# Optimization experiments

Measured on AMD Instinct MI355X. Metric: run time of the kernel, lower is better.

Reference implementation:

```python
import jax, jax.numpy as jnp
import numpy as np

NUM_EMBEDDINGS = 1024
EMBEDDING_DIM = 256
COMMITMENT_COST = 0.25


def setup_inputs() -> dict:
    key = jax.random.key(0)
    kx, ke = jax.random.split(key)
    x = jax.random.normal(kx, (8, EMBEDDING_DIM, 16, 32, 32), dtype=jnp.float32)
    emb = jax.random.uniform(ke, (NUM_EMBEDDINGS, EMBEDDING_DIM), dtype=jnp.float32,
                             minval=-1.0 / NUM_EMBEDDINGS, maxval=1.0 / NUM_EMBEDDINGS)
    return {"x": x, "emb": emb}


def reference(x, emb):
    sg = jax.lax.stop_gradient
    # x: [B, C, T, H, W] -> channels-last [B, T, H, W, C]
    x_flat = jnp.transpose(x, (0, 2, 3, 4, 1))
    flat = x_flat.reshape(-1, EMBEDDING_DIM)  # [N, D]
    # squared L2 distances to each codeword: [N, K]
    distances = (jnp.sum(flat ** 2, axis=1, keepdims=True)
                 + jnp.sum(emb ** 2, axis=1)
                 - 2.0 * flat @ emb.T)
    encoding_indices = jnp.argmin(distances, axis=1)  # [N]
    # one-hot @ codebook == direct gather
    quantized = emb[encoding_indices].reshape(x_flat.shape)
    loss = (jnp.mean((sg(quantized) - x_flat) ** 2)
            + COMMITMENT_COST * jnp.mean((quantized - sg(x_flat)) ** 2))
    # straight-through estimator
    quantized_st = x_flat + sg(quantized - x_flat)
    return jnp.transpose(quantized_st, (0, 4, 1, 2, 3)), loss
```

## Files before the change

kernel.cpp:

```cpp
#include <hip/hip_runtime.h>
#include <hip/hip_bf16.h>
#include <stdint.h>

#define N_TOT    131072
#define DIM      256
#define KCODES   1024
#define THW      16384
#define OUT_ELEMS 33554432ULL

typedef short short8 __attribute__((ext_vector_type(8)));
typedef float f32x4  __attribute__((ext_vector_type(4)));

__device__ __forceinline__ unsigned short f2bf_rne(float f) {
  union { float f; unsigned int u; } c; c.f = f;
  unsigned int u = c.u;
  unsigned int r = u + 0x7FFFu + ((u >> 16) & 1u);
  return (unsigned short)(r >> 16);
}

__device__ __forceinline__ void async_cp16(void* lds, const void* gsrc) {
  __builtin_amdgcn_global_load_lds(
      (const __attribute__((address_space(1))) void*)gsrc,
      (__attribute__((address_space(3))) void*)lds, 16, 0, 0);
}

__global__ __launch_bounds__(64) void k_prep(const float* __restrict__ emb,
                                             unsigned short* __restrict__ embB,
                                             float* __restrict__ e2) {
  const int k = blockIdx.x;
  const int t = threadIdx.x;
  const float4 v = ((const float4*)(emb + (size_t)k * DIM))[t];
  float s = v.x * v.x + v.y * v.y + v.z * v.z + v.w * v.w;
  ushort4 bv;
  bv.x = f2bf_rne(v.x); bv.y = f2bf_rne(v.y);
  bv.z = f2bf_rne(v.z); bv.w = f2bf_rne(v.w);
  const int c0 = 4 * t;
  const int ks = c0 >> 5, q = (c0 >> 3) & 3, j0 = c0 & 7;
  const int lane = q * 16 + (k & 15);
  unsigned short* dst = embB + (size_t)((((k >> 4) * 8 + ks) * 64 + lane) * 8 + j0);
  *(ushort4*)dst = bv;
  #pragma unroll
  for (int m = 32; m; m >>= 1) s += __shfl_xor(s, m, 64);
  if (t == 0) e2[k] = s;
}

__global__ __launch_bounds__(256) void k_gemm_argmin(
    const float* __restrict__ x, const unsigned short* __restrict__ embB,
    const float* __restrict__ e2, int* __restrict__ idxOut,
    float* __restrict__ lossPart) {
  __shared__ __align__(16) unsigned short eT[2][8192];
  __shared__ __align__(16) float e2l[KCODES];
  __shared__ float red[4];

  const int tid  = threadIdx.x;
  const int wave = tid >> 6;
  const int lane = tid & 63;
  const int q    = lane >> 4;
  const int l15  = lane & 15;
  const int nw0  = blockIdx.x * 128 + wave * 32;
  const int b    = nw0 >> 14;

  async_cp16((char*)e2l + tid * 16, (const char*)e2 + tid * 16);
  {
    const char* gsrc = (const char*)embB;
    char* ldst = (char*)&eT[0][0];
    #pragma unroll
    for (int kk = 0; kk < 4; ++kk)
      async_cp16(ldst + (tid + kk * 256) * 16, gsrc + (size_t)(tid + kk * 256) * 16);
  }

  short8 A[2][8];
  float x2sum = 0.0f;
  #pragma unroll
  for (int mf = 0; mf < 2; ++mf) {
    const int n   = nw0 + mf * 16 + l15;
    const int thw = n & (THW - 1);
    const float* __restrict__ xr = x + (size_t)b * DIM * THW + thw;
    #pragma unroll
    for (int ks = 0; ks < 8; ++ks) {
      const int c0 = ks * 32 + q * 8;
      short8 a;
      #pragma unroll
      for (int j = 0; j < 8; ++j) {
        float v = xr[(size_t)(c0 + j) * THW];
        x2sum += v * v;
        a[j] = (short)f2bf_rne(-2.0f * v);
      }
      A[mf][ks] = a;
    }
  }

  float pmin[2][4];
  #pragma unroll
  for (int mf = 0; mf < 2; ++mf)
    #pragma unroll
    for (int r = 0; r < 4; ++r) pmin[mf][r] = 3.4e38f;

  __syncthreads();

  for (int ch = 0; ch < 32; ++ch) {
    if (ch + 1 < 32) {
      const char* gsrc = (const char*)embB + (size_t)(ch + 1) * 16384;
      char* ldst = (char*)&eT[(ch + 1) & 1][0];
      #pragma unroll
      for (int kk = 0; kk < 4; ++kk)
        async_cp16(ldst + (tid + kk * 256) * 16, gsrc + (size_t)(tid + kk * 256) * 16);
    }
    const unsigned short* __restrict__ buf = &eT[ch & 1][0];
    const int cb = ch * 32;

    #pragma unroll
    for (int cgl = 0; cgl < 2; ++cgl) {
      short8 B[8];
      #pragma unroll
      for (int ks = 0; ks < 8; ++ks)
        B[ks] = *(const short8*)(buf + (size_t)(((cgl * 8 + ks) * 64 + lane) * 8));
      const int   cod = cb + cgl * 16 + l15;
      const float e2v = e2l[cod];

      f32x4 acc0 = {0.f, 0.f, 0.f, 0.f};
      f32x4 acc1 = {0.f, 0.f, 0.f, 0.f};
      #pragma unroll
      for (int ks = 0; ks < 8; ++ks) {
        acc0 = __builtin_amdgcn_mfma_f32_16x16x32_bf16(A[0][ks], B[ks], acc0, 0, 0, 0);
        acc1 = __builtin_amdgcn_mfma_f32_16x16x32_bf16(A[1][ks], B[ks], acc1, 0, 0, 0);
      }
      const unsigned int codu = (unsigned int)cod;
      #pragma unroll
      for (int r = 0; r < 4; ++r) {
        float d0 = acc0[r] + e2v;
        unsigned int u0 = (__float_as_uint(d0) & 0xFFFFFC00u) | codu;
        pmin[0][r] = fminf(pmin[0][r], __uint_as_float(u0));
        float d1 = acc1[r] + e2v;
        unsigned int u1 = (__float_as_uint(d1) & 0xFFFFFC00u) | codu;
        pmin[1][r] = fminf(pmin[1][r], __uint_as_float(u1));
      }
    }
    __syncthreads();
  }

  #pragma unroll
  for (int m = 1; m <= 8; m <<= 1)
    #pragma unroll
    for (int mf = 0; mf < 2; ++mf)
      #pragma unroll
      for (int r = 0; r < 4; ++r)
        pmin[mf][r] = fminf(pmin[mf][r], __shfl_xor(pmin[mf][r], m, 64));

  float sstar = 0.0f;
  if (l15 == 0) {
    #pragma unroll
    for (int mf = 0; mf < 2; ++mf)
      #pragma unroll
      for (int r = 0; r < 4; ++r) {
        const unsigned int u = __float_as_uint(pmin[mf][r]);
        idxOut[nw0 + mf * 16 + q * 4 + r] = (int)(u & 1023u);
        sstar += __uint_as_float(u & 0xFFFFFC00u);
      }
  }
  float tot = x2sum + sstar;
  #pragma unroll
  for (int m = 32; m; m >>= 1) tot += __shfl_xor(tot, m, 64);
  if (lane == 0) red[wave] = tot;
  __syncthreads();
  if (tid == 0) lossPart[blockIdx.x] = red[0] + red[1] + red[2] + red[3];
}

#define TSTR 33
__global__ __launch_bounds__(256) void k_out(
    const float* __restrict__ emb, const int* __restrict__ idx,
    float* __restrict__ out, const float* __restrict__ lossPart) {
  __shared__ __align__(16) float tile[256 * TSTR];
  const int tid  = threadIdx.x;
  const int wave = tid >> 6;
  const int lane = tid & 63;
  const int l15  = lane & 15;
  const int n0   = blockIdx.x * 256;

  if (blockIdx.x == 0 && tid < 64) {
    float s = 0.0f;
    #pragma unroll
    for (int i = 0; i < 16; ++i) s += lossPart[tid + i * 64];
    #pragma unroll
    for (int m = 32; m; m >>= 1) s += __shfl_xor(s, m, 64);
    if (tid == 0) out[OUT_ELEMS] = 1.25f * s * (1.0f / (float)OUT_ELEMS);
  }

  const int myid = idx[n0 + tid];
  const int b    = n0 >> 14;
  const int thw0 = n0 & (THW - 1);
  float* __restrict__ ob = out + (size_t)b * DIM * THW + thw0;
  const float* __restrict__ er = emb + (size_t)myid * DIM;

  for (int cc = 0; cc < 8; ++cc) {
    const int c0 = cc * 32;
    #pragma unroll
    for (int j = 0; j < 8; ++j) {
      const float4 v = *(const float4*)(er + c0 + 4 * j);
      *(float4*)&tile[tid * TSTR + 4 * j] = v;
    }
    __syncthreads();
    #pragma unroll
    for (int ci = 0; ci < 8; ++ci) {
      const int dc = (lane >> 4) + 4 * ci;
      const int nl = wave * 64 + 4 * l15;
      float4 v;
      v.x = tile[(nl + 0) * TSTR + dc];
      v.y = tile[(nl + 1) * TSTR + dc];
      v.z = tile[(nl + 2) * TSTR + dc];
      v.w = tile[(nl + 3) * TSTR + dc];
      *(float4*)(ob + (size_t)(c0 + dc) * THW + nl) = v;
    }
    __syncthreads();
  }
}

extern "C" void kernel_launch(void* const* d_in, const int* in_sizes, int n_in,
                              void* d_out, int out_size, void* d_ws, size_t ws_size,
                              hipStream_t stream) {
  const float* x   = (const float*)d_in[0];
  const float* emb = (const float*)d_in[1];
  float* out = (float*)d_out;
  char* ws = (char*)d_ws;

  unsigned short* embB = (unsigned short*)(ws);
  float* e2      = (float*)(ws + 524288);
  int*   idx     = (int*)(ws + 528384);
  float* lossPart = (float*)(ws + 1052672);

  k_prep<<<KCODES, 64, 0, stream>>>(emb, embB, e2);
  k_gemm_argmin<<<N_TOT / 128, 256, 0, stream>>>(x, embB, e2, idx, lossPart);
  k_out<<<N_TOT / 256, 256, 0, stream>>>(emb, idx, out, lossPart);
}
```

Baseline: 370.7 us.

## Pre-convert x to bf16 MFMA fragment layout in separate kernel, use output as scratch

Adds a k_xprep kernel that reads x with coalesced float4 loads, converts it to bf16 (scaled by -2), transposes it through LDS into the MFMA A-fragment layout, and stores it into the output buffer as scratch. It also computes the x^2 partial sums. The GEMM kernel then loads its A fragments with 16-byte vector reads instead of strided scalar float loads. B fragments are now loaded inside the ks loop to lower register pressure, and k_out stages 64 channels per LDS tile instead of 32. The cost is an extra kernel launch plus a round trip of bf16 x through global memory, and k_out uses more shared memory per block.

```diff
diff --git a/kernel.cpp b/kernel.cpp
--- a/kernel.cpp
+++ b/kernel.cpp
@@ -44,8 +44,66 @@
   if (t == 0) e2[k] = s;
 }
 
+__global__ __launch_bounds__(1024) void k_xprep(const float* __restrict__ x,
+                                                unsigned short* __restrict__ xf,
+                                                float* __restrict__ lossPartX) {
+  __shared__ __align__(16) unsigned short sm[64 * 264];
+  __shared__ float xred[16];
+  const int tid  = threadIdx.x;
+  const int w    = tid >> 6;
+  const int l    = tid & 63;
+  const int n0   = blockIdx.x << 8;
+  const int b    = n0 >> 14;
+  const int thw0 = n0 & (THW - 1);
+  const float* __restrict__ xb = x + (size_t)b * DIM * THW;
+  float x2 = 0.0f;
+
+  for (int q4 = 0; q4 < 4; ++q4) {
+    ushort4 bv[4];
+    #pragma unroll
+    for (int i = 0; i < 4; ++i) {
+      const int c = q4 * 64 + w * 4 + i;
+      const float4 v = *(const float4*)(xb + (size_t)c * THW + thw0 + 4 * l);
+      x2 += v.x * v.x + v.y * v.y + v.z * v.z + v.w * v.w;
+      bv[i].x = f2bf_rne(-2.0f * v.x); bv[i].y = f2bf_rne(-2.0f * v.y);
+      bv[i].z = f2bf_rne(-2.0f * v.z); bv[i].w = f2bf_rne(-2.0f * v.w);
+    }
+    if (q4) __syncthreads();
+    #pragma unroll
+    for (int i = 0; i < 4; ++i) {
+      const int cc = w * 4 + i;
+      *(ushort4*)&sm[cc * 264 + 4 * l] = bv[i];
+    }
+    __syncthreads();
+    const int oo = tid >> 7;
+    const int t2 = tid & 127;
+    unsigned int r[8];
+    #pragma unroll
+    for (int j = 0; j < 8; ++j)
+      r[j] = *(const unsigned int*)&sm[(oo * 8 + j) * 264 + 2 * t2];
+    uint4 u0, u1;
+    u0.x = (r[0] & 0xFFFFu) | (r[1] << 16);  u1.x = (r[0] >> 16) | (r[1] & 0xFFFF0000u);
+    u0.y = (r[2] & 0xFFFFu) | (r[3] << 16);  u1.y = (r[2] >> 16) | (r[3] & 0xFFFF0000u);
+    u0.z = (r[4] & 0xFFFFu) | (r[5] << 16);  u1.z = (r[4] >> 16) | (r[5] & 0xFFFF0000u);
+    u0.w = (r[6] & 0xFFFFu) | (r[7] << 16);  u1.w = (r[6] >> 16) | (r[7] & 0xFFFF0000u);
+    const size_t ui = ((size_t)blockIdx.x * 32 + (size_t)(q4 * 8 + oo)) * 256 + 2 * t2;
+    ((uint4*)xf)[ui]     = u0;
+    ((uint4*)xf)[ui + 1] = u1;
+  }
+  #pragma unroll
+  for (int m = 32; m; m >>= 1) x2 += __shfl_xor(x2, m, 64);
+  if (l == 0) xred[w] = x2;
+  __syncthreads();
+  if (tid == 0) {
+    float s = 0.0f;
+    #pragma unroll
+    for (int i = 0; i < 16; ++i) s += xred[i];
+    lossPartX[blockIdx.x] = s;
+  }
+}
+
 __global__ __launch_bounds__(256) void k_gemm_argmin(
-    const float* __restrict__ x, const unsigned short* __restrict__ embB,
+    const unsigned short* __restrict__ xf, const unsigned short* __restrict__ embB,
     const float* __restrict__ e2, int* __restrict__ idxOut,
     float* __restrict__ lossPart) {
   __shared__ __align__(16) unsigned short eT[2][8192];
@@ -58,7 +116,6 @@
   const int q    = lane >> 4;
   const int l15  = lane & 15;
   const int nw0  = blockIdx.x * 128 + wave * 32;
-  const int b    = nw0 >> 14;
 
   async_cp16((char*)e2l + tid * 16, (const char*)e2 + tid * 16);
   {
@@ -69,26 +126,15 @@
       async_cp16(ldst + (tid + kk * 256) * 16, gsrc + (size_t)(tid + kk * 256) * 16);
   }
 
+  const int tile = nw0 >> 8;
+  const int nnb  = nw0 & 255;
   short8 A[2][8];
-  float x2sum = 0.0f;
-  #pragma unroll
-  for (int mf = 0; mf < 2; ++mf) {
-    const int n   = nw0 + mf * 16 + l15;
-    const int thw = n & (THW - 1);
-    const float* __restrict__ xr = x + (size_t)b * DIM * THW + thw;
-    #pragma unroll
-    for (int ks = 0; ks < 8; ++ks) {
-      const int c0 = ks * 32 + q * 8;
-      short8 a;
-      #pragma unroll
-      for (int j = 0; j < 8; ++j) {
-        float v = xr[(size_t)(c0 + j) * THW];
-        x2sum += v * v;
-        a[j] = (short)f2bf_rne(-2.0f * v);
-      }
-      A[mf][ks] = a;
-    }
-  }
+  #pragma unroll
+  for (int mf = 0; mf < 2; ++mf)
+    #pragma unroll
+    for (int ks = 0; ks < 8; ++ks)
+      A[mf][ks] = *(const short8*)(xf +
+          (((size_t)tile * 32 + (size_t)(ks * 4 + q)) * 256 + nnb + mf * 16 + l15) * 8);
 
   float pmin[2][4];
   #pragma unroll
@@ -111,19 +157,15 @@
 
     #pragma unroll
     for (int cgl = 0; cgl < 2; ++cgl) {
-      short8 B[8];
-      #pragma unroll
-      for (int ks = 0; ks < 8; ++ks)
-        B[ks] = *(const short8*)(buf + (size_t)(((cgl * 8 + ks) * 64 + lane) * 8));
       const int   cod = cb + cgl * 16 + l15;
       const float e2v = e2l[cod];
-
       f32x4 acc0 = {0.f, 0.f, 0.f, 0.f};
       f32x4 acc1 = {0.f, 0.f, 0.f, 0.f};
       #pragma unroll
       for (int ks = 0; ks < 8; ++ks) {
-        acc0 = __builtin_amdgcn_mfma_f32_16x16x32_bf16(A[0][ks], B[ks], acc0, 0, 0, 0);
-        acc1 = __builtin_amdgcn_mfma_f32_16x16x32_bf16(A[1][ks], B[ks], acc1, 0, 0, 0);
+        const short8 Bk = *(const short8*)(buf + (size_t)(((cgl * 8 + ks) * 64 + lane) * 8));
+        acc0 = __builtin_amdgcn_mfma_f32_16x16x32_bf16(A[0][ks], Bk, acc0, 0, 0, 0);
+        acc1 = __builtin_amdgcn_mfma_f32_16x16x32_bf16(A[1][ks], Bk, acc1, 0, 0, 0);
       }
       const unsigned int codu = (unsigned int)cod;
       #pragma unroll
@@ -158,7 +200,7 @@
         sstar += __uint_as_float(u & 0xFFFFFC00u);
       }
   }
-  float tot = x2sum + sstar;
+  float tot = sstar;
   #pragma unroll
   for (int m = 32; m; m >>= 1) tot += __shfl_xor(tot, m, 64);
   if (lane == 0) red[wave] = tot;
@@ -166,10 +208,11 @@
   if (tid == 0) lossPart[blockIdx.x] = red[0] + red[1] + red[2] + red[3];
 }
 
-#define TSTR 33
+#define TSTR 65
 __global__ __launch_bounds__(256) void k_out(
     const float* __restrict__ emb, const int* __restrict__ idx,
-    float* __restrict__ out, const float* __restrict__ lossPart) {
+    float* __restrict__ out, const float* __restrict__ lossPart,
+    const float* __restrict__ lossPartX) {
   __shared__ __align__(16) float tile[256 * TSTR];
   const int tid  = threadIdx.x;
   const int wave = tid >> 6;
@@ -182,6 +225,8 @@
     #pragma unroll
     for (int i = 0; i < 16; ++i) s += lossPart[tid + i * 64];
     #pragma unroll
+    for (int i = 0; i < 8; ++i) s += lossPartX[tid + i * 64];
+    #pragma unroll
     for (int m = 32; m; m >>= 1) s += __shfl_xor(s, m, 64);
     if (tid == 0) out[OUT_ELEMS] = 1.25f * s * (1.0f / (float)OUT_ELEMS);
   }
@@ -192,16 +237,16 @@
   float* __restrict__ ob = out + (size_t)b * DIM * THW + thw0;
   const float* __restrict__ er = emb + (size_t)myid * DIM;
 
-  for (int cc = 0; cc < 8; ++cc) {
-    const int c0 = cc * 32;
-    #pragma unroll
-    for (int j = 0; j < 8; ++j) {
+  for (int cc = 0; cc < 4; ++cc) {
+    const int c0 = cc * 64;
+    #pragma unroll
+    for (int j = 0; j < 16; ++j) {
       const float4 v = *(const float4*)(er + c0 + 4 * j);
       *(float4*)&tile[tid * TSTR + 4 * j] = v;
     }
     __syncthreads();
     #pragma unroll
-    for (int ci = 0; ci < 8; ++ci) {
+    for (int ci = 0; ci < 16; ++ci) {
       const int dc = (lane >> 4) + 4 * ci;
       const int nl = wave * 64 + 4 * l15;
       float4 v;
@@ -224,11 +269,14 @@
   char* ws = (char*)d_ws;
 
   unsigned short* embB = (unsigned short*)(ws);
-  float* e2      = (float*)(ws + 524288);
-  int*   idx     = (int*)(ws + 528384);
-  float* lossPart = (float*)(ws + 1052672);
+  float* e2       = (float*)(ws + 524288);
+  int*   idx      = (int*)(ws + 528384);
+  float* lossPart  = (float*)(ws + 1052672);
+  float* lossPartX = (float*)(ws + 1056768);
+  unsigned short* xf = (unsigned short*)out;
 
   k_prep<<<KCODES, 64, 0, stream>>>(emb, embB, e2);
-  k_gemm_argmin<<<N_TOT / 128, 256, 0, stream>>>(x, embB, e2, idx, lossPart);
-  k_out<<<N_TOT / 256, 256, 0, stream>>>(emb, idx, out, lossPart);
-}
+  k_xprep<<<N_TOT / 256, 1024, 0, stream>>>(x, xf, lossPartX);
+  k_gemm_argmin<<<N_TOT / 128, 256, 0, stream>>>(xf, embB, e2, idx, lossPart);
+  k_out<<<N_TOT / 256, 256, 0, stream>>>(emb, idx, out, lossPart, lossPartX);
+}
```

Result: faster. 329.9 us (-11.0%).
